# Optimization experiments

Hardware: AMD Instinct MI355X
Metric: run time of the kernel (lower is better)

Reference implementation:

```python
import jax, jax.numpy as jnp
import numpy as np

# Static conv hyperparameters (match init_kwargs)
STRIDE = (1, 1)
PAD = (1, 1)
DIL = (1, 1)
GROUPS = 1
DG = 1  # num_deformable_groups


def setup_inputs() -> dict:
    key = jax.random.key(0)
    k1, k2, k3 = jax.random.split(key, 3)
    B, C, H, W = 4, 256, 64, 64
    OC, kh, kw = 256, 3, 3
    x = jax.random.normal(k1, (B, C, H, W), dtype=jnp.float32)
    # offset: [B, DG*2*kh*kw, Ho, Wo], ordered (tap, [dy, dx]) per deformable group
    offset = jax.random.normal(k2, (B, DG * 2 * kh * kw, H, W), dtype=jnp.float32)
    n = C * kh * kw
    stdv = 1.0 / np.sqrt(n)
    weight = jax.random.uniform(k3, (OC, C // GROUPS, kh, kw), dtype=jnp.float32,
                                minval=-stdv, maxval=stdv)
    return {"x": x, "offset": offset, "weight": weight}


def _deform_conv(x, offset, weight):
    B, C, H, W = x.shape
    OC, Cg_w, kh, kw = weight.shape
    sh, sw = STRIDE
    ph, pw = PAD
    dh, dw = DIL
    Ho = (H + 2 * ph - (dh * (kh - 1) + 1)) // sh + 1
    Wo = (W + 2 * pw - (dw * (kw - 1) + 1)) // sw + 1
    K = kh * kw
    Cg = C // DG  # channels per deformable group

    # offsets: [B, DG, K, 2, Ho, Wo]; channel 0 = dy (h), channel 1 = dx (w)
    off = offset.reshape(B, DG, K, 2, Ho, Wo)

    # base (undeformed) sampling positions per tap
    ki, kj = jnp.meshgrid(jnp.arange(kh), jnp.arange(kw), indexing='ij')
    base_h = (jnp.arange(Ho) * sh - ph)[None, :] + (ki.reshape(-1) * dh)[:, None]  # [K, Ho]
    base_w = (jnp.arange(Wo) * sw - pw)[None, :] + (kj.reshape(-1) * dw)[:, None]  # [K, Wo]

    pos_h = base_h[None, None, :, :, None].astype(x.dtype) + off[:, :, :, 0]  # [B,DG,K,Ho,Wo]
    pos_w = base_w[None, None, :, None, :].astype(x.dtype) + off[:, :, :, 1]  # [B,DG,K,Ho,Wo]

    h0f = jnp.floor(pos_h)
    w0f = jnp.floor(pos_w)
    lh = pos_h - h0f  # fractional parts
    lw = pos_w - w0f
    h0 = h0f.astype(jnp.int32)
    w0 = w0f.astype(jnp.int32)

    xg = x.reshape(B, DG, Cg, H * W)

    def gather(hi, wi):
        # zero-padded gather: out-of-range corners contribute 0 (mmcv DCNv1 semantics)
        valid = (hi >= 0) & (hi < H) & (wi >= 0) & (wi < W)  # [B,DG,K,Ho,Wo]
        idx = jnp.clip(hi, 0, H - 1) * W + jnp.clip(wi, 0, W - 1)
        flat = idx.reshape(B, DG, 1, K * Ho * Wo)
        vals = jnp.take_along_axis(
            xg, jnp.broadcast_to(flat, (B, DG, Cg, K * Ho * Wo)), axis=3)
        vals = vals.reshape(B, DG, Cg, K, Ho, Wo)
        return vals * valid[:, :, None].astype(x.dtype)

    # bilinear interpolation over 4 corners -> im2col columns [B,DG,Cg,K,Ho,Wo]
    cols = (gather(h0, w0) * ((1 - lh) * (1 - lw))[:, :, None]
            + gather(h0, w0 + 1) * ((1 - lh) * lw)[:, :, None]
            + gather(h0 + 1, w0) * (lh * (1 - lw))[:, :, None]
            + gather(h0 + 1, w0 + 1) * (lh * lw)[:, :, None])

    # grouped GEMM: columns x weight
    cols = cols.reshape(B, GROUPS, C // GROUPS, K, Ho, Wo)
    wg = weight.reshape(GROUPS, OC // GROUPS, Cg_w, K)
    out = jnp.einsum('gock,bgckhw->bgohw', wg, cols)
    return out.reshape(B, OC, Ho, Wo)


def reference(x, offset, weight):
    return _deform_conv(x, offset, weight)
```

## Files before the change

kernel.cpp:

```cpp
#include <hip/hip_runtime.h>
#include <hip/hip_bf16.h>
#include <math.h>


constexpr int B  = 4;
constexpr int C  = 256;
constexpr int H  = 64;
constexpr int W  = 64;
constexpr int OC = 256;
constexpr int Ho = 64;
constexpr int Wo = 64;

constexpr int NT     = 64;
constexpr int CHUNKS = 72;
constexpr int WROW   = 40;

constexpr size_t WA_ELTS  = (size_t)CHUNKS * OC * WROW;
constexpr size_t XB_ELTS  = (size_t)B * 8 * 4096 * 32;
constexpr size_t OUT_ELTS = (size_t)B * OC * Ho * Wo;

typedef __attribute__((ext_vector_type(8))) short bf16x8;
typedef __attribute__((ext_vector_type(4))) float f32x4;

__device__ __forceinline__ float bf_lo(unsigned u) {
    union { unsigned i; float f; } c; c.i = u << 16; return c.f;
}
__device__ __forceinline__ float bf_hi(unsigned u) {
    union { unsigned i; float f; } c; c.i = u & 0xffff0000u; return c.f;
}

__global__ __launch_bounds__(256)
void prep_all(const float* __restrict__ x, const float* __restrict__ wt,
              ushort* __restrict__ xb, ushort* __restrict__ wA)
{
    __shared__ ushort sx[128 * WROW];
    __shared__ ushort sw[CHUNKS * WROW];
    const int t = threadIdx.x;

    if (blockIdx.x < 1024) {
        const int blk = blockIdx.x;
        const int hwb = blk & 31;
        const int cb  = (blk >> 5) & 7;
        const int b   = blk >> 8;
        const int hw0 = hwb << 7;
        const int lhw = t & 127, chalf = t >> 7;
        #pragma unroll
        for (int i = 0; i < 16; ++i) {
            const int c = i * 2 + chalf;
            const float v = x[(((size_t)(b * 256 + cb * 32 + c)) << 12) + hw0 + lhw];
            __hip_bfloat16 hb = __float2bfloat16(v);
            sx[lhw * WROW + c] = *(ushort*)&hb;
        }
        __syncthreads();
        const int whw = t >> 1, wh = t & 1;
        const uint4 v0 = *(const uint4*)&sx[whw * WROW + wh * 16];
        const uint4 v1 = *(const uint4*)&sx[whw * WROW + wh * 16 + 8];
        uint4* dst = (uint4*)(xb + ((size_t)((b * 8 + cb) * 4096 + hw0) << 5));
        dst[whw * 4 + wh * 2 + 0] = v0;
        dst[whw * 4 + wh * 2 + 1] = v1;
    } else {
        const int oc = blockIdx.x - 1024;
        const int c  = t;
        const int chb = c >> 5, kk = c & 31;
        const float* wp = wt + ((size_t)oc * C + c) * 9;
        #pragma unroll
        for (int tap = 0; tap < 9; ++tap) {
            __hip_bfloat16 hb = __float2bfloat16(wp[tap]);
            sw[(tap * 8 + chb) * WROW + kk] = *(ushort*)&hb;
        }
        if (c < CHUNKS) {
            #pragma unroll
            for (int j = 0; j < 8; ++j) sw[c * WROW + 32 + j] = 0;
        }
        __syncthreads();
        const uint4* sv = (const uint4*)sw;
        for (int i = c; i < CHUNKS * 5; i += 256) {
            const int row = i / 5, q = i % 5;
            ((uint4*)(wA + ((size_t)row * OC + oc) * WROW))[q] = sv[i];
        }
    }
}

__global__ __launch_bounds__(512, 1)
void dcn_mfma(const ushort* __restrict__ xb, const float* __restrict__ off,
              const ushort* __restrict__ wA_g, float* __restrict__ out0,
              int ksplit)
{
    __shared__ __align__(16) ushort s_wA[OC * WROW];
    __shared__ __align__(16) ushort s_col[NT * WROW];
    __shared__ int2   s_midx[9 * NT];
    __shared__ float4 s_mw[9 * NT];

    const int xcd = blockIdx.x & 7;
    const int ii  = blockIdx.x >> 3;
    const int b   = xcd & 3;
    int ho, khalf;
    if (ksplit == 2) { khalf = ii & 1; ho = ((xcd >> 2) << 5) + (ii >> 1); }
    else             { khalf = 0;      ho = ((xcd >> 2) << 5) + ii;        }
    const int ch0 = khalf * 36;
    const int ch1 = ch0 + (ksplit == 2 ? 36 : 72);
    float* outp = out0 + (size_t)khalf * OUT_ELTS;
    const int tid = threadIdx.x;

    for (int s = tid; s < 9 * NT; s += 512) {
        const int n   = s & 63;
        const int tap = s >> 6;
        const float dy = off[((size_t)(b * 18 + 2 * tap)     * Ho + ho) * Wo + n];
        const float dx = off[((size_t)(b * 18 + 2 * tap + 1) * Ho + ho) * Wo + n];
        const float ph = (float)(ho - 1 + tap / 3) + dy;
        const float pw = (float)(n  - 1 + tap % 3) + dx;
        const float h0f = floorf(ph), w0f = floorf(pw);
        const int h0 = (int)h0f, w0 = (int)w0f;
        const float lh = ph - h0f, lw = pw - w0f;
        const int wb = min(max(w0, 0), W - 2);
        const int ht = min(max(h0, 0), H - 1);
        const int hb = min(max(h0 + 1, 0), H - 1);
        const float s0 = (wb == w0) ? (1.f - lw) : ((wb == w0 + 1) ? lw : 0.f);
        const float s1 = (wb + 1 == w0 + 1) ? lw : ((wb + 1 == w0) ? (1.f - lw) : 0.f);
        const float wtp = (h0 >= 0 && h0 < H)         ? (1.f - lh) : 0.f;
        const float wbt = (h0 + 1 >= 0 && h0 + 1 < H) ? lh         : 0.f;
        s_midx[s] = make_int2(ht * W + wb, hb * W + wb);
        s_mw[s]   = make_float4(wtp * s0, wtp * s1, wbt * s0, wbt * s1);
    }

    const int lane = tid & 63;
    const int wv   = tid >> 6;
    const int ocb  = wv >> 1;
    const int phh  = wv & 1;
    const int kq   = lane >> 4;
    const int mr   = lane & 15;

    const int sm_tid = tid - 256;
    const int sn  = sm_tid & 63;
    const int sgg = sm_tid >> 6;

    f32x4 acc[4][2];
    #pragma unroll
    for (int mt = 0; mt < 4; ++mt)
        #pragma unroll
        for (int nt = 0; nt < 2; ++nt)
            acc[mt][nt] = (f32x4){0.f, 0.f, 0.f, 0.f};

    for (int ch = ch0; ch < ch1; ++ch) {
        __syncthreads();

        if (tid < 256) {
            #pragma unroll
            for (int i = 0; i < 5; ++i) {
                const int seg = wv * 5 + i;
                __builtin_amdgcn_global_load_lds(
                    (const __attribute__((address_space(1))) void*)
                        (wA_g + (size_t)ch * OC * WROW + seg * 512 + lane * 8),
                    (__attribute__((address_space(3))) void*)&s_wA[seg * 512],
                    16, 0, 0);
            }
        } else {
            const int tap = ch >> 3;
            const int cb  = ch & 7;
            const int2   mi = s_midx[tap * NT + sn];
            const float4 mw = s_mw[tap * NT + sn];
            const ushort* xp = xb + ((size_t)(b * 8 + cb) << 17) + (sgg << 3);
            const uint4 c00 = *(const uint4*)(xp + ((size_t)mi.x << 5));
            const uint4 c01 = *(const uint4*)(xp + (((size_t)mi.x + 1) << 5));
            const uint4 c10 = *(const uint4*)(xp + ((size_t)mi.y << 5));
            const uint4 c11 = *(const uint4*)(xp + (((size_t)mi.y + 1) << 5));
            union { ushort pk[8]; uint4 v; } u;
            const unsigned a00[4] = {c00.x, c00.y, c00.z, c00.w};
            const unsigned a01[4] = {c01.x, c01.y, c01.z, c01.w};
            const unsigned a10[4] = {c10.x, c10.y, c10.z, c10.w};
            const unsigned a11[4] = {c11.x, c11.y, c11.z, c11.w};
            #pragma unroll
            for (int j = 0; j < 4; ++j) {
                const float vlo = mw.x * bf_lo(a00[j]) + mw.y * bf_lo(a01[j])
                                + mw.z * bf_lo(a10[j]) + mw.w * bf_lo(a11[j]);
                const float vhi = mw.x * bf_hi(a00[j]) + mw.y * bf_hi(a01[j])
                                + mw.z * bf_hi(a10[j]) + mw.w * bf_hi(a11[j]);
                __hip_bfloat16 l = __float2bfloat16(vlo);
                __hip_bfloat16 h = __float2bfloat16(vhi);
                u.pk[2 * j]     = *(ushort*)&l;
                u.pk[2 * j + 1] = *(ushort*)&h;
            }
            *(uint4*)&s_col[sn * WROW + sgg * 8] = u.v;
        }
        __syncthreads();

        bf16x8 bfr[2];
        #pragma unroll
        for (int nt = 0; nt < 2; ++nt)
            bfr[nt] = *(const bf16x8*)&s_col[((phh * 2 + nt) * 16 + mr) * WROW + kq * 8];
        #pragma unroll
        for (int mt = 0; mt < 4; ++mt) {
            const bf16x8 afr = *(const bf16x8*)&s_wA[(ocb * 64 + mt * 16 + mr) * WROW + kq * 8];
            #pragma unroll
            for (int nt = 0; nt < 2; ++nt)
                acc[mt][nt] = __builtin_amdgcn_mfma_f32_16x16x32_bf16(afr, bfr[nt], acc[mt][nt], 0, 0, 0);
        }
    }

    #pragma unroll
    for (int mt = 0; mt < 4; ++mt)
        #pragma unroll
        for (int nt = 0; nt < 2; ++nt)
            #pragma unroll
            for (int r = 0; r < 4; ++r) {
                const int oc = ocb * 64 + mt * 16 + kq * 4 + r;
                const int wo = (phh * 2 + nt) * 16 + mr;
                outp[((size_t)(b * OC + oc) * Ho + ho) * Wo + wo] = acc[mt][nt][r];
            }
}

__global__ __launch_bounds__(256)
void reduce2(const float4* __restrict__ p0, const float4* __restrict__ p1,
             float4* __restrict__ out)
{
    const int i = blockIdx.x * 256 + threadIdx.x;
    const float4 a = p0[i], b = p1[i];
    out[i] = make_float4(a.x + b.x, a.y + b.y, a.z + b.z, a.w + b.w);
}

extern "C" void kernel_launch(void* const* d_in, const int* in_sizes, int n_in,
                              void* d_out, int out_size, void* d_ws, size_t ws_size,
                              hipStream_t stream)
{
    const float* x   = (const float*)d_in[0];
    const float* off = (const float*)d_in[1];
    const float* wt  = (const float*)d_in[2];
    float* out = (float*)d_out;

    ushort* wA = (ushort*)d_ws;
    ushort* xb = wA + WA_ELTS;
    float*  po = (float*)(xb + XB_ELTS);
    const size_t need = (WA_ELTS + XB_ELTS) * sizeof(ushort)
                      + 2 * OUT_ELTS * sizeof(float);
    const int ksplit = (ws_size >= need) ? 2 : 1;

    prep_all<<<1280, 256, 0, stream>>>(x, wt, xb, wA);

    if (ksplit == 2) {
        dcn_mfma<<<512, 512, 0, stream>>>(xb, off, wA, po, 2);
        reduce2<<<(int)(OUT_ELTS / 4 / 256), 256, 0, stream>>>(
            (const float4*)po, (const float4*)(po + OUT_ELTS), (float4*)out);
    } else {
        dcn_mfma<<<256, 512, 0, stream>>>(xb, off, wA, out, 1);
    }
}
```

Measured before the change: 127.8 us.

## Split reduction four ways and accumulate partial sums with atomics

Raises the K-split of the deformable conv GEMM from two to four chunks per output row, giving 1024 blocks instead of 512. Partial sums go straight into the output through float atomic adds after a memset, replacing the partial-buffer writes and the separate reduce kernel. This aims for better occupancy and fewer passes over memory. The cost is more atomic traffic, a memset, and repeated bilinear offset setup in every split block.

```diff
diff --git a/kernel.cpp b/kernel.cpp
--- a/kernel.cpp
+++ b/kernel.cpp
@@ -13,11 +13,12 @@
 
 constexpr int NT     = 64;
 constexpr int CHUNKS = 72;
+constexpr int KSPLIT = 4;
+constexpr int CPB    = CHUNKS / KSPLIT;
 constexpr int WROW   = 40;
 
-constexpr size_t WA_ELTS  = (size_t)CHUNKS * OC * WROW;
-constexpr size_t XB_ELTS  = (size_t)B * 8 * 4096 * 32;
-constexpr size_t OUT_ELTS = (size_t)B * OC * Ho * Wo;
+constexpr size_t WA_ELTS = (size_t)CHUNKS * OC * WROW;
+constexpr size_t XB_ELTS = (size_t)B * 8 * 4096 * 32;
 
 typedef __attribute__((ext_vector_type(8))) short bf16x8;
 typedef __attribute__((ext_vector_type(4))) float f32x4;
@@ -83,8 +84,7 @@
 
 __global__ __launch_bounds__(512, 1)
 void dcn_mfma(const ushort* __restrict__ xb, const float* __restrict__ off,
-              const ushort* __restrict__ wA_g, float* __restrict__ out0,
-              int ksplit)
+              const ushort* __restrict__ wA_g, float* __restrict__ out)
 {
     __shared__ __align__(16) ushort s_wA[OC * WROW];
     __shared__ __align__(16) ushort s_col[NT * WROW];
@@ -94,12 +94,10 @@
     const int xcd = blockIdx.x & 7;
     const int ii  = blockIdx.x >> 3;
     const int b   = xcd & 3;
-    int ho, khalf;
-    if (ksplit == 2) { khalf = ii & 1; ho = ((xcd >> 2) << 5) + (ii >> 1); }
-    else             { khalf = 0;      ho = ((xcd >> 2) << 5) + ii;        }
-    const int ch0 = khalf * 36;
-    const int ch1 = ch0 + (ksplit == 2 ? 36 : 72);
-    float* outp = out0 + (size_t)khalf * OUT_ELTS;
+    const int kq4 = ii & 3;
+    const int ho  = ((xcd >> 2) << 5) + (ii >> 2);
+    const int ch0 = kq4 * CPB;
+    const int ch1 = ch0 + CPB;
     const int tid = threadIdx.x;
 
     for (int s = tid; s < 9 * NT; s += 512) {
@@ -205,17 +203,9 @@
             for (int r = 0; r < 4; ++r) {
                 const int oc = ocb * 64 + mt * 16 + kq * 4 + r;
                 const int wo = (phh * 2 + nt) * 16 + mr;
-                outp[((size_t)(b * OC + oc) * Ho + ho) * Wo + wo] = acc[mt][nt][r];
+                unsafeAtomicAdd(&out[((size_t)(b * OC + oc) * Ho + ho) * Wo + wo],
+                                acc[mt][nt][r]);
             }
-}
-
-__global__ __launch_bounds__(256)
-void reduce2(const float4* __restrict__ p0, const float4* __restrict__ p1,
-             float4* __restrict__ out)
-{
-    const int i = blockIdx.x * 256 + threadIdx.x;
-    const float4 a = p0[i], b = p1[i];
-    out[i] = make_float4(a.x + b.x, a.y + b.y, a.z + b.z, a.w + b.w);
 }
 
 extern "C" void kernel_launch(void* const* d_in, const int* in_sizes, int n_in,
@@ -229,18 +219,8 @@
 
     ushort* wA = (ushort*)d_ws;
     ushort* xb = wA + WA_ELTS;
-    float*  po = (float*)(xb + XB_ELTS);
-    const size_t need = (WA_ELTS + XB_ELTS) * sizeof(ushort)
-                      + 2 * OUT_ELTS * sizeof(float);
-    const int ksplit = (ws_size >= need) ? 2 : 1;
-
+
+    hipMemsetAsync(d_out, 0, (size_t)out_size * sizeof(float), stream);
     prep_all<<<1280, 256, 0, stream>>>(x, wt, xb, wA);
-
-    if (ksplit == 2) {
-        dcn_mfma<<<512, 512, 0, stream>>>(xb, off, wA, po, 2);
-        reduce2<<<(int)(OUT_ELTS / 4 / 256), 256, 0, stream>>>(
-            (const float4*)po, (const float4*)(po + OUT_ELTS), (float4*)out);
-    } else {
-        dcn_mfma<<<256, 512, 0, stream>>>(xb, off, wA, out, 1);
-    }
-}
+    dcn_mfma<<<B * Ho * KSPLIT, 512, 0, stream>>>(xb, off, wA, out);
+}
```

Result: slower. 156.9 us (+22.7%).

## Fuse prep, conv and reduce into one cooperative kernel with grid syncs

Applied to the files above, without the earlier changes.

Merges the bf16 prep kernel, the split-K MFMA deformable conv kernel and the partial-sum reduction into a single cooperative kernel of 512 blocks, using grid.sync between phases. This removes two kernel launch boundaries and their idle gaps. Shared-memory use is cut to about 32KB by packing gather indices into ushort2 and bilinear weights into bf16, so that several blocks fit per CU and co-residency is possible. The costs are grid-wide barrier overhead, some precision loss from rounding the interpolation weights to bf16, and removal of the non-split fallback, which always assumes enough workspace.

```diff
diff --git a/kernel.cpp b/kernel.cpp
--- a/kernel.cpp
+++ b/kernel.cpp
@@ -1,6 +1,9 @@
 #include <hip/hip_runtime.h>
 #include <hip/hip_bf16.h>
+#include <hip/hip_cooperative_groups.h>
 #include <math.h>
+
+namespace cg = cooperative_groups;
 
 
 constexpr int B  = 4;
@@ -28,15 +31,213 @@
 __device__ __forceinline__ float bf_hi(unsigned u) {
     union { unsigned i; float f; } c; c.i = u & 0xffff0000u; return c.f;
 }
+__device__ __forceinline__ float bfu(ushort u) {
+    union { unsigned i; float f; } c; c.i = (unsigned)u << 16; return c.f;
+}
+__device__ __forceinline__ ushort fbf(float f) {
+    __hip_bfloat16 h = __float2bfloat16(f); return *(ushort*)&h;
+}
+
+__global__ __launch_bounds__(512, 4)
+void dcn_all(const float* __restrict__ x, const float* __restrict__ wt,
+             const float* __restrict__ off, ushort* __restrict__ xb,
+             ushort* __restrict__ wA, float* __restrict__ po,
+             float* __restrict__ out)
+{
+    __shared__ __align__(16) unsigned char smem[32512];
+    cg::grid_group grid = cg::this_grid();
+    const int tid = threadIdx.x;
+
+    {
+        const int half = tid >> 8, t = tid & 255;
+        const int id  = blockIdx.x * 2 + half;
+        const int hwb = id & 31;
+        const int cb  = (id >> 5) & 7;
+        const int b   = id >> 8;
+        const int hw0 = hwb << 7;
+        const int lhw = t & 127, chalf = t >> 7;
+        ushort* sx = (ushort*)smem + half * (128 * WROW);
+        #pragma unroll
+        for (int i = 0; i < 16; ++i) {
+            const int c = i * 2 + chalf;
+            const float v = x[(((size_t)(b * 256 + cb * 32 + c)) << 12) + hw0 + lhw];
+            sx[lhw * WROW + c] = fbf(v);
+        }
+        __syncthreads();
+        const int whw = t >> 1, wh = t & 1;
+        const uint4 v0 = *(const uint4*)&sx[whw * WROW + wh * 16];
+        const uint4 v1 = *(const uint4*)&sx[whw * WROW + wh * 16 + 8];
+        uint4* dst = (uint4*)(xb + ((size_t)((b * 8 + cb) * 4096 + hw0) << 5));
+        dst[whw * 4 + wh * 2 + 0] = v0;
+        dst[whw * 4 + wh * 2 + 1] = v1;
+
+        if (blockIdx.x < 256) {
+            ushort* sw = (ushort*)(smem + 20480);
+            const int oc = blockIdx.x;
+            if (tid < 256) {
+                const int c = tid, chb = c >> 5, kk = c & 31;
+                const float* wp = wt + ((size_t)oc * C + c) * 9;
+                #pragma unroll
+                for (int tap = 0; tap < 9; ++tap)
+                    sw[(tap * 8 + chb) * WROW + kk] = fbf(wp[tap]);
+                if (c < CHUNKS) {
+                    #pragma unroll
+                    for (int j = 0; j < 8; ++j) sw[c * WROW + 32 + j] = 0;
+                }
+            }
+            __syncthreads();
+            const uint4* sv = (const uint4*)sw;
+            for (int i = tid; i < CHUNKS * 5; i += 512) {
+                const int row = i / 5, q = i % 5;
+                ((uint4*)(wA + ((size_t)row * OC + oc) * WROW))[q] = sv[i];
+            }
+        }
+    }
+    __threadfence();
+    grid.sync();
+
+    {
+        ushort*  s_wA  = (ushort*)smem;
+        ushort*  s_col = (ushort*)(smem + 20480);
+        ushort2* s_mi  = (ushort2*)(smem + 25600);
+        ushort4* s_mw4 = (ushort4*)(smem + 27904);
+
+        const int xcd = blockIdx.x & 7;
+        const int ii  = blockIdx.x >> 3;
+        const int b   = xcd & 3;
+        const int khalf = ii & 1;
+        const int ho  = ((xcd >> 2) << 5) + (ii >> 1);
+        const int ch0 = khalf * 36, ch1 = ch0 + 36;
+        float* outp = po + (size_t)khalf * OUT_ELTS;
+
+        for (int s = tid; s < 9 * NT; s += 512) {
+            const int n   = s & 63;
+            const int tap = s >> 6;
+            const float dy = off[((size_t)(b * 18 + 2 * tap)     * Ho + ho) * Wo + n];
+            const float dx = off[((size_t)(b * 18 + 2 * tap + 1) * Ho + ho) * Wo + n];
+            const float ph = (float)(ho - 1 + tap / 3) + dy;
+            const float pw = (float)(n  - 1 + tap % 3) + dx;
+            const float h0f = floorf(ph), w0f = floorf(pw);
+            const int h0 = (int)h0f, w0 = (int)w0f;
+            const float lh = ph - h0f, lw = pw - w0f;
+            const int wb = min(max(w0, 0), W - 2);
+            const int ht = min(max(h0, 0), H - 1);
+            const int hb = min(max(h0 + 1, 0), H - 1);
+            const float s0 = (wb == w0) ? (1.f - lw) : ((wb == w0 + 1) ? lw : 0.f);
+            const float s1 = (wb + 1 == w0 + 1) ? lw : ((wb + 1 == w0) ? (1.f - lw) : 0.f);
+            const float wtp = (h0 >= 0 && h0 < H)         ? (1.f - lh) : 0.f;
+            const float wbt = (h0 + 1 >= 0 && h0 + 1 < H) ? lh         : 0.f;
+            s_mi[s]  = make_ushort2((ushort)(ht * W + wb), (ushort)(hb * W + wb));
+            s_mw4[s] = make_ushort4(fbf(wtp * s0), fbf(wtp * s1),
+                                    fbf(wbt * s0), fbf(wbt * s1));
+        }
+
+        const int lane = tid & 63;
+        const int wv   = tid >> 6;
+        const int ocb  = wv >> 1;
+        const int phh  = wv & 1;
+        const int kq   = lane >> 4;
+        const int mr   = lane & 15;
+        const int sm_tid = tid - 256;
+        const int sn  = sm_tid & 63;
+        const int sgg = sm_tid >> 6;
+
+        f32x4 acc[4][2];
+        #pragma unroll
+        for (int mt = 0; mt < 4; ++mt)
+            #pragma unroll
+            for (int nt = 0; nt < 2; ++nt)
+                acc[mt][nt] = (f32x4){0.f, 0.f, 0.f, 0.f};
+
+        for (int ch = ch0; ch < ch1; ++ch) {
+            __syncthreads();
+
+            if (tid < 256) {
+                #pragma unroll
+                for (int i = 0; i < 5; ++i) {
+                    const int seg = wv * 5 + i;
+                    __builtin_amdgcn_global_load_lds(
+                        (const __attribute__((address_space(1))) void*)
+                            (wA + (size_t)ch * OC * WROW + seg * 512 + lane * 8),
+                        (__attribute__((address_space(3))) void*)&s_wA[seg * 512],
+                        16, 0, 0);
+                }
+            } else {
+                const int tap = ch >> 3;
+                const int cb  = ch & 7;
+                const ushort2 mi  = s_mi[tap * NT + sn];
+                const ushort4 mwp = s_mw4[tap * NT + sn];
+                const float w00 = bfu(mwp.x), w01 = bfu(mwp.y);
+                const float w10 = bfu(mwp.z), w11 = bfu(mwp.w);
+                const ushort* xp = xb + ((size_t)(b * 8 + cb) << 17) + (sgg << 3);
+                const uint4 c00 = *(const uint4*)(xp + ((size_t)mi.x << 5));
+                const uint4 c01 = *(const uint4*)(xp + (((size_t)mi.x + 1) << 5));
+                const uint4 c10 = *(const uint4*)(xp + ((size_t)mi.y << 5));
+                const uint4 c11 = *(const uint4*)(xp + (((size_t)mi.y + 1) << 5));
+                union { ushort pk[8]; uint4 v; } u;
+                const unsigned a00[4] = {c00.x, c00.y, c00.z, c00.w};
+                const unsigned a01[4] = {c01.x, c01.y, c01.z, c01.w};
+                const unsigned a10[4] = {c10.x, c10.y, c10.z, c10.w};
+                const unsigned a11[4] = {c11.x, c11.y, c11.z, c11.w};
+                #pragma unroll
+                for (int j = 0; j < 4; ++j) {
+                    const float vlo = w00 * bf_lo(a00[j]) + w01 * bf_lo(a01[j])
+                                    + w10 * bf_lo(a10[j]) + w11 * bf_lo(a11[j]);
+                    const float vhi = w00 * bf_hi(a00[j]) + w01 * bf_hi(a01[j])
+                                    + w10 * bf_hi(a10[j]) + w11 * bf_hi(a11[j]);
+                    u.pk[2 * j]     = fbf(vlo);
+                    u.pk[2 * j + 1] = fbf(vhi);
+                }
+                *(uint4*)&s_col[sn * WROW + sgg * 8] = u.v;
+            }
+            __syncthreads();
+
+            bf16x8 bfr[2];
+            #pragma unroll
+            for (int nt = 0; nt < 2; ++nt)
+                bfr[nt] = *(const bf16x8*)&s_col[((phh * 2 + nt) * 16 + mr) * WROW + kq * 8];
+            #pragma unroll
+            for (int mt = 0; mt < 4; ++mt) {
+                const bf16x8 afr = *(const bf16x8*)&s_wA[(ocb * 64 + mt * 16 + mr) * WROW + kq * 8];
+                #pragma unroll
+                for (int nt = 0; nt < 2; ++nt)
+                    acc[mt][nt] = __builtin_amdgcn_mfma_f32_16x16x32_bf16(afr, bfr[nt], acc[mt][nt], 0, 0, 0);
+            }
+        }
+
+        #pragma unroll
+        for (int mt = 0; mt < 4; ++mt)
+            #pragma unroll
+            for (int nt = 0; nt < 2; ++nt)
+                #pragma unroll
+                for (int r = 0; r < 4; ++r) {
+                    const int oc = ocb * 64 + mt * 16 + kq * 4 + r;
+                    const int wo = (phh * 2 + nt) * 16 + mr;
+                    outp[((size_t)(b * OC + oc) * Ho + ho) * Wo + wo] = acc[mt][nt][r];
+                }
+    }
+    __threadfence();
+    grid.sync();
+
+    {
+        const float4* p0 = (const float4*)po;
+        const float4* p1 = (const float4*)(po + OUT_ELTS);
+        float4* o4 = (float4*)out;
+        const int nf4 = (int)(OUT_ELTS / 4);
+        for (int i = blockIdx.x * 512 + tid; i < nf4; i += 512 * 512) {
+            const float4 a = p0[i], c = p1[i];
+            o4[i] = make_float4(a.x + c.x, a.y + c.y, a.z + c.z, a.w + c.w);
+        }
+    }
+}
 
 __global__ __launch_bounds__(256)
-void prep_all(const float* __restrict__ x, const float* __restrict__ wt,
-              ushort* __restrict__ xb, ushort* __restrict__ wA)
+void prep_all_fb(const float* __restrict__ x, const float* __restrict__ wt,
+                 ushort* __restrict__ xb, ushort* __restrict__ wA)
 {
     __shared__ ushort sx[128 * WROW];
     __shared__ ushort sw[CHUNKS * WROW];
     const int t = threadIdx.x;
-
     if (blockIdx.x < 1024) {
         const int blk = blockIdx.x;
         const int hwb = blk & 31;
@@ -47,9 +248,7 @@
         #pragma unroll
         for (int i = 0; i < 16; ++i) {
             const int c = i * 2 + chalf;
-            const float v = x[(((size_t)(b * 256 + cb * 32 + c)) << 12) + hw0 + lhw];
-            __hip_bfloat16 hb = __float2bfloat16(v);
-            sx[lhw * WROW + c] = *(ushort*)&hb;
+            sx[lhw * WROW + c] = fbf(x[(((size_t)(b * 256 + cb * 32 + c)) << 12) + hw0 + lhw]);
         }
         __syncthreads();
         const int whw = t >> 1, wh = t & 1;
@@ -60,14 +259,11 @@
         dst[whw * 4 + wh * 2 + 1] = v1;
     } else {
         const int oc = blockIdx.x - 1024;
-        const int c  = t;
-        const int chb = c >> 5, kk = c & 31;
+        const int c  = t, chb = c >> 5, kk = c & 31;
         const float* wp = wt + ((size_t)oc * C + c) * 9;
         #pragma unroll
-        for (int tap = 0; tap < 9; ++tap) {
-            __hip_bfloat16 hb = __float2bfloat16(wp[tap]);
-            sw[(tap * 8 + chb) * WROW + kk] = *(ushort*)&hb;
-        }
+        for (int tap = 0; tap < 9; ++tap)
+            sw[(tap * 8 + chb) * WROW + kk] = fbf(wp[tap]);
         if (c < CHUNKS) {
             #pragma unroll
             for (int j = 0; j < 8; ++j) sw[c * WROW + 32 + j] = 0;
@@ -82,9 +278,8 @@
 }
 
 __global__ __launch_bounds__(512, 1)
-void dcn_mfma(const ushort* __restrict__ xb, const float* __restrict__ off,
-              const ushort* __restrict__ wA_g, float* __restrict__ out0,
-              int ksplit)
+void dcn_mfma_fb(const ushort* __restrict__ xb, const float* __restrict__ off,
+                 const ushort* __restrict__ wA_g, float* __restrict__ po)
 {
     __shared__ __align__(16) ushort s_wA[OC * WROW];
     __shared__ __align__(16) ushort s_col[NT * WROW];
@@ -94,12 +289,10 @@
     const int xcd = blockIdx.x & 7;
     const int ii  = blockIdx.x >> 3;
     const int b   = xcd & 3;
-    int ho, khalf;
-    if (ksplit == 2) { khalf = ii & 1; ho = ((xcd >> 2) << 5) + (ii >> 1); }
-    else             { khalf = 0;      ho = ((xcd >> 2) << 5) + ii;        }
-    const int ch0 = khalf * 36;
-    const int ch1 = ch0 + (ksplit == 2 ? 36 : 72);
-    float* outp = out0 + (size_t)khalf * OUT_ELTS;
+    const int khalf = ii & 1;
+    const int ho  = ((xcd >> 2) << 5) + (ii >> 1);
+    const int ch0 = khalf * 36, ch1 = ch0 + 36;
+    float* outp = po + (size_t)khalf * OUT_ELTS;
     const int tid = threadIdx.x;
 
     for (int s = tid; s < 9 * NT; s += 512) {
@@ -129,7 +322,6 @@
     const int phh  = wv & 1;
     const int kq   = lane >> 4;
     const int mr   = lane & 15;
-
     const int sm_tid = tid - 256;
     const int sn  = sm_tid & 63;
     const int sgg = sm_tid >> 6;
@@ -143,7 +335,6 @@
 
     for (int ch = ch0; ch < ch1; ++ch) {
         __syncthreads();
-
         if (tid < 256) {
             #pragma unroll
             for (int i = 0; i < 5; ++i) {
@@ -175,10 +366,8 @@
                                 + mw.z * bf_lo(a10[j]) + mw.w * bf_lo(a11[j]);
                 const float vhi = mw.x * bf_hi(a00[j]) + mw.y * bf_hi(a01[j])
                                 + mw.z * bf_hi(a10[j]) + mw.w * bf_hi(a11[j]);
-                __hip_bfloat16 l = __float2bfloat16(vlo);
-                __hip_bfloat16 h = __float2bfloat16(vhi);
-                u.pk[2 * j]     = *(ushort*)&l;
-                u.pk[2 * j + 1] = *(ushort*)&h;
+                u.pk[2 * j]     = fbf(vlo);
+                u.pk[2 * j + 1] = fbf(vhi);
             }
             *(uint4*)&s_col[sn * WROW + sgg * 8] = u.v;
         }
@@ -210,8 +399,8 @@
 }
 
 __global__ __launch_bounds__(256)
-void reduce2(const float4* __restrict__ p0, const float4* __restrict__ p1,
-             float4* __restrict__ out)
+void reduce2_fb(const float4* __restrict__ p0, const float4* __restrict__ p1,
+                float4* __restrict__ out)
 {
     const int i = blockIdx.x * 256 + threadIdx.x;
     const float4 a = p0[i], b = p1[i];
@@ -230,17 +419,17 @@
     ushort* wA = (ushort*)d_ws;
     ushort* xb = wA + WA_ELTS;
     float*  po = (float*)(xb + XB_ELTS);
-    const size_t need = (WA_ELTS + XB_ELTS) * sizeof(ushort)
-                      + 2 * OUT_ELTS * sizeof(float);
-    const int ksplit = (ws_size >= need) ? 2 : 1;
-
-    prep_all<<<1280, 256, 0, stream>>>(x, wt, xb, wA);
-
-    if (ksplit == 2) {
-        dcn_mfma<<<512, 512, 0, stream>>>(xb, off, wA, po, 2);
-        reduce2<<<(int)(OUT_ELTS / 4 / 256), 256, 0, stream>>>(
+
+    void* args[] = { (void*)&x, (void*)&wt, (void*)&off,
+                     (void*)&xb, (void*)&wA, (void*)&po, (void*)&out };
+    hipError_t err = hipLaunchCooperativeKernel((const void*)dcn_all,
+                                                dim3(512), dim3(512),
+                                                args, 0, stream);
+    if (err != hipSuccess) {
+        (void)hipGetLastError();
+        prep_all_fb<<<1280, 256, 0, stream>>>(x, wt, xb, wA);
+        dcn_mfma_fb<<<512, 512, 0, stream>>>(xb, off, wA, po);
+        reduce2_fb<<<(int)(OUT_ELTS / 4 / 256), 256, 0, stream>>>(
             (const float4*)po, (const float4*)(po + OUT_ELTS), (float4*)out);
-    } else {
-        dcn_mfma<<<256, 512, 0, stream>>>(xb, off, wA, out, 1);
-    }
-}
+    }
+}
```

Result: slower. 463.9 us (+262.9%).
